# Performance work log

Hardware: AMD Instinct MI355X
Metric: run time of the kernel (lower is better)

## Reference

```python
import jax, jax.numpy as jnp
import numpy as np

DROPOUT_P = 0.5


def spmm(edge_weight, src, dst, x, n_nodes):
    # out[i] = sum_{e: dst[e]==i} edge_weight[e] * x[src[e]]  == spmm(adj, x)
    msgs = x[src] * edge_weight[:, None]          # [E, F]
    return jax.ops.segment_sum(msgs, dst, num_segments=n_nodes)


def setup_inputs() -> dict:
    key = jax.random.key(0)
    ks = jax.random.split(key, 7)
    N, E, F_IN, F_HID, F_OUT = 100000, 1600000, 128, 128, 64
    return {
        "x": jax.random.normal(ks[0], (N, F_IN), dtype=jnp.float32),
        "edge_weight": jax.random.uniform(ks[1], (E,), dtype=jnp.float32),
        "W1": jax.random.normal(ks[2], (F_IN, F_HID), dtype=jnp.float32) * 0.05,
        "b1": jnp.zeros((F_HID,), dtype=jnp.float32),
        "W2": jax.random.normal(ks[3], (F_HID, F_OUT), dtype=jnp.float32) * 0.05,
        "b2": jnp.zeros((F_OUT,), dtype=jnp.float32),
        "src": jax.random.randint(ks[4], (E,), 0, N, dtype=jnp.int32),
        "dst": jax.random.randint(ks[5], (E,), 0, N, dtype=jnp.int32),
        "n_nodes": N,
    }


def reference(x, edge_weight, W1, b1, W2, b2, src, dst, n_nodes):
    # layer 1: relu(Linear(spmm(adj, x)))
    h = spmm(edge_weight, src, dst, x, n_nodes)
    h = jax.nn.relu(h @ W1 + b1)
    # dropout (training=True), deterministic fixed key for reproducibility
    keep = jax.random.bernoulli(jax.random.key(42), 1.0 - DROPOUT_P, h.shape)
    h = jnp.where(keep, h / (1.0 - DROPOUT_P), 0.0)
    # layer 2: Linear(spmm(adj, h))
    h = spmm(edge_weight, src, dst, h, n_nodes)
    return h @ W2 + b2
```

## Files before the change

### kernel.cpp

```cpp
#include <hip/hip_runtime.h>

typedef unsigned int u32;
typedef unsigned short u16;
typedef __attribute__((ext_vector_type(8))) short short8;
typedef __attribute__((ext_vector_type(8))) unsigned short u16x8;
typedef __attribute__((ext_vector_type(4))) float f32x4;
typedef __attribute__((ext_vector_type(4))) unsigned short u16x4;

#define CAP 4864
#define EPB 8192

__device__ __forceinline__ u16 f2bf(float f) {
  u32 u = __builtin_bit_cast(u32, f);
  u32 r = (u + 0x7fffu + ((u >> 16) & 1u)) >> 16;
  return (u16)r;
}
__device__ __forceinline__ float bf2f(u32 lo16) {
  return __builtin_bit_cast(float, lo16 << 16);
}

__device__ __forceinline__ void threefry2x32(u32 k0, u32 k1, u32 x0, u32 x1,
                                             u32& y0, u32& y1) {
  const u32 ks2 = k0 ^ k1 ^ 0x1BD11BDAu;
#define TFR(r) { x0 += x1; x1 = (x1 << (r)) | (x1 >> (32 - (r))); x1 ^= x0; }
  x0 += k0; x1 += k1;
  TFR(13) TFR(15) TFR(26) TFR(6)
  x0 += k1; x1 += ks2 + 1u;
  TFR(17) TFR(29) TFR(16) TFR(24)
  x0 += ks2; x1 += k0 + 2u;
  TFR(13) TFR(15) TFR(26) TFR(6)
  x0 += k0; x1 += k1 + 3u;
  TFR(17) TFR(29) TFR(16) TFR(24)
  x0 += k1; x1 += ks2 + 4u;
  TFR(13) TFR(15) TFR(26) TFR(6)
  x0 += ks2; x1 += k0 + 5u;
#undef TFR
  y0 = x0; y1 = x1;
}

__device__ __forceinline__ bool dropout_keep(u32 j) {
  u32 y0, y1;
  threefry2x32(0u, 42u, 0u, j, y0, y1);
  return ((y0 ^ y1) & 0x80000000u) == 0u;
}

__global__ __launch_bounds__(256) void gemmA_stage_fused(
    const float* __restrict__ X, const float* __restrict__ W,
    u16* __restrict__ Y, int N, int cBlocks,
    const int* __restrict__ src, const int* __restrict__ dst,
    const float* __restrict__ ew, int* __restrict__ bcur,
    int2* __restrict__ staged, int E, int nb) {
  __shared__ short As[128 * 128];
  __shared__ short Bs[128 * 128];
  const int t = threadIdx.x;

  if (blockIdx.x < cBlocks) {
    int* h  = (int*)As;
    int* cb = ((int*)As) + 512;
    for (int j = t; j < nb; j += 256) h[j] = 0;
    __syncthreads();
    const int base = blockIdx.x * EPB;
    const int end = min(base + EPB, E);
    for (int i = base + t; i < end; i += 256)
      atomicAdd(&h[(u32)dst[i] >> 8], 1);
    __syncthreads();
    for (int j = t; j < nb; j += 256) {
      cb[j] = h[j] ? atomicAdd(&bcur[j], h[j]) : 0;
      h[j] = 0;
    }
    __syncthreads();
    for (int i = base + t; i < end; i += 256) {
      int d = dst[i];
      int b = (u32)d >> 8;
      int loc = atomicAdd(&h[b], 1);
      int pos = cb[b] + loc;
      if (pos < CAP)
        staged[(size_t)b * CAP + pos] =
            make_int2(src[i] | ((d & 255) << 23), __builtin_bit_cast(int, ew[i]));
    }
    return;
  }

  const int row0 = (blockIdx.x - cBlocks) << 7;

  for (int i = t; i < 128 * 32; i += 256) {
    int m = i >> 5, k4 = i & 31;
    int r = row0 + m;
    float4 v = make_float4(0.f, 0.f, 0.f, 0.f);
    if (r < N) v = reinterpret_cast<const float4*>(X)[(size_t)r * 32 + k4];
    u16x4 b;
    b.x = f2bf(v.x); b.y = f2bf(v.y); b.z = f2bf(v.z); b.w = f2bf(v.w);
    int off = (m * 128 + (k4 << 2)) ^ ((m & 7) << 3);
    *reinterpret_cast<u16x4*>(&As[off]) = b;
  }
  for (int i = t; i < 128 * 32; i += 256) {
    int k = i >> 5, n4 = i & 31;
    float4 v = reinterpret_cast<const float4*>(W)[(size_t)k * 32 + n4];
    int c0 = n4 << 2;
    Bs[(((c0 + 0) * 128 + k)) ^ (((c0 + 0) & 7) << 3)] = (short)f2bf(v.x);
    Bs[(((c0 + 1) * 128 + k)) ^ (((c0 + 1) & 7) << 3)] = (short)f2bf(v.y);
    Bs[(((c0 + 2) * 128 + k)) ^ (((c0 + 2) & 7) << 3)] = (short)f2bf(v.z);
    Bs[(((c0 + 3) * 128 + k)) ^ (((c0 + 3) & 7) << 3)] = (short)f2bf(v.w);
  }
  __syncthreads();

  const int wid = t >> 6, lane = t & 63;
  const int wr = (wid >> 1) * 64, wc = (wid & 1) * 64;
  const int l15 = lane & 15, lk = (lane >> 4) * 8;

  f32x4 acc[4][4];
#pragma unroll
  for (int m = 0; m < 4; ++m)
#pragma unroll
    for (int n = 0; n < 4; ++n) acc[m][n] = (f32x4)(0.f);

#pragma unroll
  for (int kk = 0; kk < 4; ++kk) {
    const int kb = kk * 32 + lk;
    short8 a[4], b[4];
#pragma unroll
    for (int m = 0; m < 4; ++m) {
      int row = wr + m * 16 + l15;
      a[m] = *reinterpret_cast<const short8*>(&As[(row * 128 + kb) ^ ((row & 7) << 3)]);
    }
#pragma unroll
    for (int n = 0; n < 4; ++n) {
      int col = wc + n * 16 + l15;
      b[n] = *reinterpret_cast<const short8*>(&Bs[(col * 128 + kb) ^ ((col & 7) << 3)]);
    }
#pragma unroll
    for (int m = 0; m < 4; ++m)
#pragma unroll
      for (int n = 0; n < 4; ++n)
        acc[m][n] = __builtin_amdgcn_mfma_f32_16x16x32_bf16(a[m], b[n], acc[m][n], 0, 0, 0);
  }

#pragma unroll
  for (int m = 0; m < 4; ++m) {
    int rbase = row0 + wr + m * 16 + (lane >> 4) * 4;
#pragma unroll
    for (int n = 0; n < 4; ++n) {
      int col = wc + n * 16 + l15;
#pragma unroll
      for (int r = 0; r < 4; ++r) {
        int row = rbase + r;
        if (row < N) Y[(size_t)row * 128 + col] = f2bf(acc[m][n][r]);
      }
    }
  }
}

__global__ __launch_bounds__(256) void bucket_sort(
    const int2* __restrict__ staged, const int* __restrict__ bcur,
    int2* __restrict__ rowinfo, int2* __restrict__ epk, int N) {
  __shared__ int cnt[256];
  __shared__ int cur[256];
  __shared__ int sc[256];
  const int t = threadIdx.x;
  const int b = blockIdx.x;
  const int node0 = b << 8;
  const int nn = min(256, N - node0);
  const int ebase = b * CAP;
  const int ecnt = min(bcur[b], CAP);
  cnt[t] = 0;
  __syncthreads();
  for (int i = t; i < ecnt; i += 256)
    atomicAdd(&cnt[(u32)staged[ebase + i].x >> 23], 1);
  __syncthreads();
  int a = cnt[t];
  int pa = (a + 1) & ~1;
  sc[t] = pa;
  __syncthreads();
  for (int off = 1; off < 256; off <<= 1) {
    int tmp = (t >= off) ? sc[t - off] : 0;
    __syncthreads();
    sc[t] += tmp;
    __syncthreads();
  }
  int excl = sc[t] - pa;
  cur[t] = ebase + excl;
  if (t < nn) rowinfo[node0 + t] = make_int2(ebase + excl, a);
  __syncthreads();
  for (int i = t; i < ecnt; i += 256) {
    int2 p = staged[ebase + i];
    int dl = (u32)p.x >> 23;
    int pos = atomicAdd(&cur[dl], 1);
    epk[pos] = make_int2(p.x & 0x7fffff, p.y);
  }
}

#define F128_FMA2(VA, VB, W0, W1)                      \
  { float w0 = __builtin_bit_cast(float, W0);          \
    float w1 = __builtin_bit_cast(float, W1);          \
    a0 = fmaf(bf2f((VA).x & 0xffffu), w0, a0);         \
    a1 = fmaf(bf2f((VA).x >> 16), w0, a1);             \
    a2 = fmaf(bf2f((VA).y & 0xffffu), w0, a2);         \
    a3 = fmaf(bf2f((VA).y >> 16), w0, a3);             \
    a0 = fmaf(bf2f((VB).x & 0xffffu), w1, a0);         \
    a1 = fmaf(bf2f((VB).x >> 16), w1, a1);             \
    a2 = fmaf(bf2f((VB).y & 0xffffu), w1, a2);         \
    a3 = fmaf(bf2f((VB).y >> 16), w1, a3); }

__global__ __launch_bounds__(256) void spmm_csr_f128_bf16(
    const u16* __restrict__ V, const int2* __restrict__ epk,
    const int2* __restrict__ rowinfo, u16* __restrict__ out, int N) {
  int node = blockIdx.x * 8 + (threadIdx.x >> 5);
  if (node >= N) return;
  int l32 = threadIdx.x & 31;
  int2 ri = rowinfo[node];
  int e = ri.x, end = ri.x + ri.y;
  float a0 = 0.f, a1 = 0.f, a2 = 0.f, a3 = 0.f;
  for (; e + 16 <= end; e += 16) {
    int4 pp[8];
#pragma unroll
    for (int k = 0; k < 8; ++k)
      pp[k] = reinterpret_cast<const int4*>(epk + e)[k];
    uint2 v[16];
#pragma unroll
    for (int k = 0; k < 8; ++k) {
      v[2 * k] = reinterpret_cast<const uint2*>(V + (size_t)pp[k].x * 128)[l32];
      v[2 * k + 1] = reinterpret_cast<const uint2*>(V + (size_t)pp[k].z * 128)[l32];
    }
#pragma unroll
    for (int k = 0; k < 8; ++k)
      F128_FMA2(v[2 * k], v[2 * k + 1], pp[k].y, pp[k].w);
  }
  for (; e + 4 <= end; e += 4) {
    int4 pp[2];
#pragma unroll
    for (int k = 0; k < 2; ++k)
      pp[k] = reinterpret_cast<const int4*>(epk + e)[k];
    uint2 v[4];
#pragma unroll
    for (int k = 0; k < 2; ++k) {
      v[2 * k] = reinterpret_cast<const uint2*>(V + (size_t)pp[k].x * 128)[l32];
      v[2 * k + 1] = reinterpret_cast<const uint2*>(V + (size_t)pp[k].z * 128)[l32];
    }
#pragma unroll
    for (int k = 0; k < 2; ++k)
      F128_FMA2(v[2 * k], v[2 * k + 1], pp[k].y, pp[k].w);
  }
  for (; e < end; ++e) {
    int2 p = epk[e];
    uint2 v = reinterpret_cast<const uint2*>(V + (size_t)p.x * 128)[l32];
    float w = __builtin_bit_cast(float, p.y);
    a0 = fmaf(bf2f(v.x & 0xffffu), w, a0);
    a1 = fmaf(bf2f(v.x >> 16), w, a1);
    a2 = fmaf(bf2f(v.y & 0xffffu), w, a2);
    a3 = fmaf(bf2f(v.y >> 16), w, a3);
  }
  uint2 o;
  o.x = (u32)f2bf(a0) | ((u32)f2bf(a1) << 16);
  o.y = (u32)f2bf(a2) | ((u32)f2bf(a3) << 16);
  reinterpret_cast<uint2*>(out + (size_t)node * 128)[l32] = o;
}

__global__ __launch_bounds__(256) void spmm_csr_f64_bias(
    const u16* __restrict__ V, const int2* __restrict__ epk,
    const int2* __restrict__ rowinfo, const float* __restrict__ b2,
    float* __restrict__ out, int N) {
  int node = blockIdx.x * 16 + (threadIdx.x >> 4);
  if (node >= N) return;
  int l16 = threadIdx.x & 15;
  int2 ri = rowinfo[node];
  int e = ri.x, end = ri.x + ri.y;
  float4 bb = reinterpret_cast<const float4*>(b2)[l16];
  float a0 = bb.x, a1 = bb.y, a2 = bb.z, a3 = bb.w;
  for (; e + 16 <= end; e += 16) {
    int4 pp[8];
#pragma unroll
    for (int k = 0; k < 8; ++k)
      pp[k] = reinterpret_cast<const int4*>(epk + e)[k];
    uint2 v[16];
#pragma unroll
    for (int k = 0; k < 8; ++k) {
      v[2 * k] = reinterpret_cast<const uint2*>(V + (size_t)pp[k].x * 64)[l16];
      v[2 * k + 1] = reinterpret_cast<const uint2*>(V + (size_t)pp[k].z * 64)[l16];
    }
#pragma unroll
    for (int k = 0; k < 8; ++k)
      F128_FMA2(v[2 * k], v[2 * k + 1], pp[k].y, pp[k].w);
  }
  for (; e + 4 <= end; e += 4) {
    int4 pp[2];
#pragma unroll
    for (int k = 0; k < 2; ++k)
      pp[k] = reinterpret_cast<const int4*>(epk + e)[k];
    uint2 v[4];
#pragma unroll
    for (int k = 0; k < 2; ++k) {
      v[2 * k] = reinterpret_cast<const uint2*>(V + (size_t)pp[k].x * 64)[l16];
      v[2 * k + 1] = reinterpret_cast<const uint2*>(V + (size_t)pp[k].z * 64)[l16];
    }
#pragma unroll
    for (int k = 0; k < 2; ++k)
      F128_FMA2(v[2 * k], v[2 * k + 1], pp[k].y, pp[k].w);
  }
  for (; e < end; ++e) {
    int2 p = epk[e];
    uint2 v = reinterpret_cast<const uint2*>(V + (size_t)p.x * 64)[l16];
    float w = __builtin_bit_cast(float, p.y);
    a0 = fmaf(bf2f(v.x & 0xffffu), w, a0);
    a1 = fmaf(bf2f(v.x >> 16), w, a1);
    a2 = fmaf(bf2f(v.y & 0xffffu), w, a2);
    a3 = fmaf(bf2f(v.y >> 16), w, a3);
  }
  reinterpret_cast<float4*>(out + (size_t)node * 64)[l16] =
      make_float4(a0, a1, a2, a3);
}

__global__ __launch_bounds__(256) void gemm_h_w2_mfma(
    const u16* __restrict__ H, const float* __restrict__ bias1,
    const float* __restrict__ W2, u16* __restrict__ O, int N) {
  __shared__ short As[128 * 128];
  __shared__ short Bs[64 * 128];
  const int t = threadIdx.x;
  const int row0 = blockIdx.x << 7;

  for (int i = t; i < 128 * 16; i += 256) {
    int k = i >> 4, n4 = i & 15;
    float4 v = reinterpret_cast<const float4*>(W2)[(size_t)k * 16 + n4];
    int c0 = n4 << 2;
    Bs[(((c0 + 0) * 128 + k)) ^ (((c0 + 0) & 7) << 3)] = (short)f2bf(v.x);
    Bs[(((c0 + 1) * 128 + k)) ^ (((c0 + 1) & 7) << 3)] = (short)f2bf(v.y);
    Bs[(((c0 + 2) * 128 + k)) ^ (((c0 + 2) & 7) << 3)] = (short)f2bf(v.z);
    Bs[(((c0 + 3) * 128 + k)) ^ (((c0 + 3) & 7) << 3)] = (short)f2bf(v.w);
  }

  for (int i = t; i < 128 * 16; i += 256) {
    int m = i >> 4, g = i & 15;
    int r = row0 + m;
    int c0 = g << 3;
    u16x8 o = (u16x8)(0);
    if (r < N) {
      u16x8 v = *reinterpret_cast<const u16x8*>(H + (size_t)r * 128 + c0);
      float4 b0 = reinterpret_cast<const float4*>(bias1)[g * 2];
      float4 b1v = reinterpret_cast<const float4*>(bias1)[g * 2 + 1];
      float bb[8] = {b0.x, b0.y, b0.z, b0.w, b1v.x, b1v.y, b1v.z, b1v.w};
      u32 base = (u32)r * 128u + (u32)c0;
#pragma unroll
      for (int e = 0; e < 8; ++e) {
        float z = fmaxf(bf2f((u16)v[e]) + bb[e], 0.f);
        o[e] = dropout_keep(base + e) ? f2bf(z + z) : (u16)0;
      }
    }
    *reinterpret_cast<u16x8*>(&As[(m * 128 + c0) ^ ((m & 7) << 3)]) = o;
  }
  __syncthreads();

  const int wid = t >> 6, lane = t & 63;
  const int wr = wid * 32;
  const int l15 = lane & 15, lk = (lane >> 4) * 8;

  f32x4 acc[2][4];
#pragma unroll
  for (int m = 0; m < 2; ++m)
#pragma unroll
    for (int n = 0; n < 4; ++n) acc[m][n] = (f32x4)(0.f);

#pragma unroll
  for (int kk = 0; kk < 4; ++kk) {
    const int kb = kk * 32 + lk;
    short8 a[2], b[4];
#pragma unroll
    for (int m = 0; m < 2; ++m) {
      int row = wr + m * 16 + l15;
      a[m] = *reinterpret_cast<const short8*>(&As[(row * 128 + kb) ^ ((row & 7) << 3)]);
    }
#pragma unroll
    for (int n = 0; n < 4; ++n) {
      int col = n * 16 + l15;
      b[n] = *reinterpret_cast<const short8*>(&Bs[(col * 128 + kb) ^ ((col & 7) << 3)]);
    }
#pragma unroll
    for (int m = 0; m < 2; ++m)
#pragma unroll
      for (int n = 0; n < 4; ++n)
        acc[m][n] = __builtin_amdgcn_mfma_f32_16x16x32_bf16(a[m], b[n], acc[m][n], 0, 0, 0);
  }

#pragma unroll
  for (int m = 0; m < 2; ++m) {
    int rbase = row0 + wr + m * 16 + (lane >> 4) * 4;
#pragma unroll
    for (int n = 0; n < 4; ++n) {
      int col = n * 16 + l15;
#pragma unroll
      for (int r = 0; r < 4; ++r) {
        int row = rbase + r;
        if (row < N) O[(size_t)row * 64 + col] = f2bf(acc[m][n][r]);
      }
    }
  }
}

extern "C" void kernel_launch(void* const* d_in, const int* in_sizes, int n_in,
                              void* d_out, int out_size, void* d_ws, size_t ws_size,
                              hipStream_t stream) {
  const float* x  = (const float*)d_in[0];
  const float* ew = (const float*)d_in[1];
  const float* W1 = (const float*)d_in[2];
  const float* b1 = (const float*)d_in[3];
  const float* W2 = (const float*)d_in[4];
  const float* b2 = (const float*)d_in[5];
  const int*   src = (const int*)d_in[6];
  const int*   dst = (const int*)d_in[7];
  const int N = in_sizes[0] / 128;
  const int E = in_sizes[1];
  float* out = (float*)d_out;

  const int nb = (N + 255) >> 8;

  u16*   h1      = (u16*)d_ws;
  u16*   y       = h1 + (size_t)N * 128;
  u16*   h3      = y;
  int2*  staged  = (int2*)(y + (size_t)N * 128);
  int2*  epk     = staged + (size_t)nb * CAP;
  int2*  rowinfo = epk + (size_t)nb * CAP;
  int*   bcur    = (int*)(rowinfo + N + 4);

  const int cBlocks = (E + EPB - 1) / EPB;
  const int gBlocks = (N + 127) / 128;

  hipMemsetAsync(bcur, 0, (size_t)nb * sizeof(int), stream);
  gemmA_stage_fused<<<cBlocks + gBlocks, 256, 0, stream>>>(
      x, W1, y, N, cBlocks, src, dst, ew, bcur, staged, E, nb);
  bucket_sort<<<nb, 256, 0, stream>>>(staged, bcur, rowinfo, epk, N);
  spmm_csr_f128_bf16<<<(N + 7) / 8, 256, 0, stream>>>(y, epk, rowinfo, h1, N);
  gemm_h_w2_mfma<<<gBlocks, 256, 0, stream>>>(h1, b1, W2, h3, N);
  spmm_csr_f64_bias<<<(N + 15) / 16, 256, 0, stream>>>(h3, epk, rowinfo, b2, out, N);
}
```

Baseline: 234.8 us.

## Split fused staging/GEMM kernel and shrink tiles for staging and W2 GEMM

Splits the combined edge-staging plus X·W1 GEMM kernel into two separate launches, so the staging blocks only reserve 4KB of shared memory instead of 64KB. This should raise occupancy for the atomic-heavy staging pass. Edges per staging block are halved, giving more blocks, and the W2 GEMM now uses 64-row tiles to launch twice as many smaller blocks with less shared memory. In exchange there is one more kernel launch, the two phases can no longer overlap within a single launch, and there are more global atomics on bucket counters.

Result: slower. 244.9 us (+4.3%).

```diff
diff --git a/kernel.cpp b/kernel.cpp
--- a/kernel.cpp
+++ b/kernel.cpp
@@ -8,7 +8,7 @@
 typedef __attribute__((ext_vector_type(4))) unsigned short u16x4;
 
 #define CAP 4864
-#define EPB 8192
+#define EPB 4096
 
 __device__ __forceinline__ u16 f2bf(float f) {
   u32 u = __builtin_bit_cast(u32, f);
@@ -44,109 +44,33 @@
   return ((y0 ^ y1) & 0x80000000u) == 0u;
 }
 
-__global__ __launch_bounds__(256) void gemmA_stage_fused(
-    const float* __restrict__ X, const float* __restrict__ W,
-    u16* __restrict__ Y, int N, int cBlocks,
+__global__ __launch_bounds__(256) void stage_edges(
     const int* __restrict__ src, const int* __restrict__ dst,
     const float* __restrict__ ew, int* __restrict__ bcur,
     int2* __restrict__ staged, int E, int nb) {
-  __shared__ short As[128 * 128];
-  __shared__ short Bs[128 * 128];
+  __shared__ int h[512];
+  __shared__ int cb[512];
   const int t = threadIdx.x;
-
-  if (blockIdx.x < cBlocks) {
-    int* h  = (int*)As;
-    int* cb = ((int*)As) + 512;
-    for (int j = t; j < nb; j += 256) h[j] = 0;
-    __syncthreads();
-    const int base = blockIdx.x * EPB;
-    const int end = min(base + EPB, E);
-    for (int i = base + t; i < end; i += 256)
-      atomicAdd(&h[(u32)dst[i] >> 8], 1);
-    __syncthreads();
-    for (int j = t; j < nb; j += 256) {
-      cb[j] = h[j] ? atomicAdd(&bcur[j], h[j]) : 0;
-      h[j] = 0;
-    }
-    __syncthreads();
-    for (int i = base + t; i < end; i += 256) {
-      int d = dst[i];
-      int b = (u32)d >> 8;
-      int loc = atomicAdd(&h[b], 1);
-      int pos = cb[b] + loc;
-      if (pos < CAP)
-        staged[(size_t)b * CAP + pos] =
-            make_int2(src[i] | ((d & 255) << 23), __builtin_bit_cast(int, ew[i]));
-    }
-    return;
-  }
-
-  const int row0 = (blockIdx.x - cBlocks) << 7;
-
-  for (int i = t; i < 128 * 32; i += 256) {
-    int m = i >> 5, k4 = i & 31;
-    int r = row0 + m;
-    float4 v = make_float4(0.f, 0.f, 0.f, 0.f);
-    if (r < N) v = reinterpret_cast<const float4*>(X)[(size_t)r * 32 + k4];
-    u16x4 b;
-    b.x = f2bf(v.x); b.y = f2bf(v.y); b.z = f2bf(v.z); b.w = f2bf(v.w);
-    int off = (m * 128 + (k4 << 2)) ^ ((m & 7) << 3);
-    *reinterpret_cast<u16x4*>(&As[off]) = b;
-  }
-  for (int i = t; i < 128 * 32; i += 256) {
-    int k = i >> 5, n4 = i & 31;
-    float4 v = reinterpret_cast<const float4*>(W)[(size_t)k * 32 + n4];
-    int c0 = n4 << 2;
-    Bs[(((c0 + 0) * 128 + k)) ^ (((c0 + 0) & 7) << 3)] = (short)f2bf(v.x);
-    Bs[(((c0 + 1) * 128 + k)) ^ (((c0 + 1) & 7) << 3)] = (short)f2bf(v.y);
-    Bs[(((c0 + 2) * 128 + k)) ^ (((c0 + 2) & 7) << 3)] = (short)f2bf(v.z);
-    Bs[(((c0 + 3) * 128 + k)) ^ (((c0 + 3) & 7) << 3)] = (short)f2bf(v.w);
-  }
-  __syncthreads();
-
-  const int wid = t >> 6, lane = t & 63;
-  const int wr = (wid >> 1) * 64, wc = (wid & 1) * 64;
-  const int l15 = lane & 15, lk = (lane >> 4) * 8;
-
-  f32x4 acc[4][4];
-#pragma unroll
-  for (int m = 0; m < 4; ++m)
-#pragma unroll
-    for (int n = 0; n < 4; ++n) acc[m][n] = (f32x4)(0.f);
-
-#pragma unroll
-  for (int kk = 0; kk < 4; ++kk) {
-    const int kb = kk * 32 + lk;
-    short8 a[4], b[4];
-#pragma unroll
-    for (int m = 0; m < 4; ++m) {
-      int row = wr + m * 16 + l15;
-      a[m] = *reinterpret_cast<const short8*>(&As[(row * 128 + kb) ^ ((row & 7) << 3)]);
-    }
-#pragma unroll
-    for (int n = 0; n < 4; ++n) {
-      int col = wc + n * 16 + l15;
-      b[n] = *reinterpret_cast<const short8*>(&Bs[(col * 128 + kb) ^ ((col & 7) << 3)]);
-    }
-#pragma unroll
-    for (int m = 0; m < 4; ++m)
-#pragma unroll
-      for (int n = 0; n < 4; ++n)
-        acc[m][n] = __builtin_amdgcn_mfma_f32_16x16x32_bf16(a[m], b[n], acc[m][n], 0, 0, 0);
-  }
-
-#pragma unroll
-  for (int m = 0; m < 4; ++m) {
-    int rbase = row0 + wr + m * 16 + (lane >> 4) * 4;
-#pragma unroll
-    for (int n = 0; n < 4; ++n) {
-      int col = wc + n * 16 + l15;
-#pragma unroll
-      for (int r = 0; r < 4; ++r) {
-        int row = rbase + r;
-        if (row < N) Y[(size_t)row * 128 + col] = f2bf(acc[m][n][r]);
-      }
-    }
+  for (int j = t; j < nb; j += 256) h[j] = 0;
+  __syncthreads();
+  const int base = blockIdx.x * EPB;
+  const int end = min(base + EPB, E);
+  for (int i = base + t; i < end; i += 256)
+    atomicAdd(&h[(u32)dst[i] >> 8], 1);
+  __syncthreads();
+  for (int j = t; j < nb; j += 256) {
+    cb[j] = h[j] ? atomicAdd(&bcur[j], h[j]) : 0;
+    h[j] = 0;
+  }
+  __syncthreads();
+  for (int i = base + t; i < end; i += 256) {
+    int d = dst[i];
+    int b = (u32)d >> 8;
+    int loc = atomicAdd(&h[b], 1);
+    int pos = cb[b] + loc;
+    if (pos < CAP)
+      staged[(size_t)b * CAP + pos] =
+          make_int2(src[i] | ((d & 255) << 23), __builtin_bit_cast(int, ew[i]));
   }
 }
 
@@ -309,13 +233,88 @@
       make_float4(a0, a1, a2, a3);
 }
 
+__global__ __launch_bounds__(256) void gemm_xw1_mfma(
+    const float* __restrict__ X, const float* __restrict__ W,
+    u16* __restrict__ Y, int N) {
+  __shared__ short As[128 * 128];
+  __shared__ short Bs[128 * 128];
+  const int t = threadIdx.x;
+  const int row0 = blockIdx.x << 7;
+
+  for (int i = t; i < 128 * 32; i += 256) {
+    int m = i >> 5, k4 = i & 31;
+    int r = row0 + m;
+    float4 v = make_float4(0.f, 0.f, 0.f, 0.f);
+    if (r < N) v = reinterpret_cast<const float4*>(X)[(size_t)r * 32 + k4];
+    u16x4 b;
+    b.x = f2bf(v.x); b.y = f2bf(v.y); b.z = f2bf(v.z); b.w = f2bf(v.w);
+    int off = (m * 128 + (k4 << 2)) ^ ((m & 7) << 3);
+    *reinterpret_cast<u16x4*>(&As[off]) = b;
+  }
+  for (int i = t; i < 128 * 32; i += 256) {
+    int k = i >> 5, n4 = i & 31;
+    float4 v = reinterpret_cast<const float4*>(W)[(size_t)k * 32 + n4];
+    int c0 = n4 << 2;
+    Bs[(((c0 + 0) * 128 + k)) ^ (((c0 + 0) & 7) << 3)] = (short)f2bf(v.x);
+    Bs[(((c0 + 1) * 128 + k)) ^ (((c0 + 1) & 7) << 3)] = (short)f2bf(v.y);
+    Bs[(((c0 + 2) * 128 + k)) ^ (((c0 + 2) & 7) << 3)] = (short)f2bf(v.z);
+    Bs[(((c0 + 3) * 128 + k)) ^ (((c0 + 3) & 7) << 3)] = (short)f2bf(v.w);
+  }
+  __syncthreads();
+
+  const int wid = t >> 6, lane = t & 63;
+  const int wr = (wid >> 1) * 64, wc = (wid & 1) * 64;
+  const int l15 = lane & 15, lk = (lane >> 4) * 8;
+
+  f32x4 acc[4][4];
+#pragma unroll
+  for (int m = 0; m < 4; ++m)
+#pragma unroll
+    for (int n = 0; n < 4; ++n) acc[m][n] = (f32x4)(0.f);
+
+#pragma unroll
+  for (int kk = 0; kk < 4; ++kk) {
+    const int kb = kk * 32 + lk;
+    short8 a[4], b[4];
+#pragma unroll
+    for (int m = 0; m < 4; ++m) {
+      int row = wr + m * 16 + l15;
+      a[m] = *reinterpret_cast<const short8*>(&As[(row * 128 + kb) ^ ((row & 7) << 3)]);
+    }
+#pragma unroll
+    for (int n = 0; n < 4; ++n) {
+      int col = wc + n * 16 + l15;
+      b[n] = *reinterpret_cast<const short8*>(&Bs[(col * 128 + kb) ^ ((col & 7) << 3)]);
+    }
+#pragma unroll
+    for (int m = 0; m < 4; ++m)
+#pragma unroll
+      for (int n = 0; n < 4; ++n)
+        acc[m][n] = __builtin_amdgcn_mfma_f32_16x16x32_bf16(a[m], b[n], acc[m][n], 0, 0, 0);
+  }
+
+#pragma unroll
+  for (int m = 0; m < 4; ++m) {
+    int rbase = row0 + wr + m * 16 + (lane >> 4) * 4;
+#pragma unroll
+    for (int n = 0; n < 4; ++n) {
+      int col = wc + n * 16 + l15;
+#pragma unroll
+      for (int r = 0; r < 4; ++r) {
+        int row = rbase + r;
+        if (row < N) Y[(size_t)row * 128 + col] = f2bf(acc[m][n][r]);
+      }
+    }
+  }
+}
+
 __global__ __launch_bounds__(256) void gemm_h_w2_mfma(
     const u16* __restrict__ H, const float* __restrict__ bias1,
     const float* __restrict__ W2, u16* __restrict__ O, int N) {
-  __shared__ short As[128 * 128];
+  __shared__ short As[64 * 128];
   __shared__ short Bs[64 * 128];
   const int t = threadIdx.x;
-  const int row0 = blockIdx.x << 7;
+  const int row0 = blockIdx.x << 6;
 
   for (int i = t; i < 128 * 16; i += 256) {
     int k = i >> 4, n4 = i & 15;
@@ -327,7 +326,7 @@
     Bs[(((c0 + 3) * 128 + k)) ^ (((c0 + 3) & 7) << 3)] = (short)f2bf(v.w);
   }
 
-  for (int i = t; i < 128 * 16; i += 256) {
+  for (int i = t; i < 64 * 16; i += 256) {
     int m = i >> 4, g = i & 15;
     int r = row0 + m;
     int c0 = g << 3;
@@ -349,46 +348,38 @@
   __syncthreads();
 
   const int wid = t >> 6, lane = t & 63;
-  const int wr = wid * 32;
+  const int wr = wid * 16;
   const int l15 = lane & 15, lk = (lane >> 4) * 8;
 
-  f32x4 acc[2][4];
-#pragma unroll
-  for (int m = 0; m < 2; ++m)
-#pragma unroll
-    for (int n = 0; n < 4; ++n) acc[m][n] = (f32x4)(0.f);
+  f32x4 acc[4];
+#pragma unroll
+  for (int n = 0; n < 4; ++n) acc[n] = (f32x4)(0.f);
 
 #pragma unroll
   for (int kk = 0; kk < 4; ++kk) {
     const int kb = kk * 32 + lk;
-    short8 a[2], b[4];
-#pragma unroll
-    for (int m = 0; m < 2; ++m) {
-      int row = wr + m * 16 + l15;
-      a[m] = *reinterpret_cast<const short8*>(&As[(row * 128 + kb) ^ ((row & 7) << 3)]);
-    }
+    int row = wr + l15;
+    short8 a = *reinterpret_cast<const short8*>(&As[(row * 128 + kb) ^ ((row & 7) << 3)]);
+    short8 b[4];
 #pragma unroll
     for (int n = 0; n < 4; ++n) {
       int col = n * 16 + l15;
       b[n] = *reinterpret_cast<const short8*>(&Bs[(col * 128 + kb) ^ ((col & 7) << 3)]);
     }
 #pragma unroll
-    for (int m = 0; m < 2; ++m)
-#pragma unroll
-      for (int n = 0; n < 4; ++n)
-        acc[m][n] = __builtin_amdgcn_mfma_f32_16x16x32_bf16(a[m], b[n], acc[m][n], 0, 0, 0);
-  }
-
-#pragma unroll
-  for (int m = 0; m < 2; ++m) {
-    int rbase = row0 + wr + m * 16 + (lane >> 4) * 4;
+    for (int n = 0; n < 4; ++n)
+      acc[n] = __builtin_amdgcn_mfma_f32_16x16x32_bf16(a, b[n], acc[n], 0, 0, 0);
+  }
+
+  {
+    int rbase = row0 + wr + (lane >> 4) * 4;
 #pragma unroll
     for (int n = 0; n < 4; ++n) {
       int col = n * 16 + l15;
 #pragma unroll
       for (int r = 0; r < 4; ++r) {
         int row = rbase + r;
-        if (row < N) O[(size_t)row * 64 + col] = f2bf(acc[m][n][r]);
+        if (row < N) O[(size_t)row * 64 + col] = f2bf(acc[n][r]);
       }
     }
   }
@@ -423,10 +414,10 @@
   const int gBlocks = (N + 127) / 128;
 
   hipMemsetAsync(bcur, 0, (size_t)nb * sizeof(int), stream);
-  gemmA_stage_fused<<<cBlocks + gBlocks, 256, 0, stream>>>(
-      x, W1, y, N, cBlocks, src, dst, ew, bcur, staged, E, nb);
+  stage_edges<<<cBlocks, 256, 0, stream>>>(src, dst, ew, bcur, staged, E, nb);
+  gemm_xw1_mfma<<<gBlocks, 256, 0, stream>>>(x, W1, y, N);
   bucket_sort<<<nb, 256, 0, stream>>>(staged, bcur, rowinfo, epk, N);
   spmm_csr_f128_bf16<<<(N + 7) / 8, 256, 0, stream>>>(y, epk, rowinfo, h1, N);
-  gemm_h_w2_mfma<<<gBlocks, 256, 0, stream>>>(h1, b1, W2, h3, N);
+  gemm_h_w2_mfma<<<(N + 63) / 64, 256, 0, stream>>>(h1, b1, W2, h3, N);
   spmm_csr_f64_bias<<<(N + 15) / 16, 256, 0, stream>>>(h3, epk, rowinfo, b2, out, N);
 }
```
